# Kernel optimization log

Hardware: AMD Instinct MI355X
Metric: run time of the kernel (lower is better)

The kernel has to match this reference:

```python
import jax, jax.numpy as jnp
import numpy as np

D_IN, D_K, D_V, N_HEADS = 1024, 64, 64, 16
B, S = 4, 2048


def setup_inputs() -> dict:
    key = jax.random.key(0)
    ks = jax.random.split(key, 9)
    scale = 1.0 / np.sqrt(D_IN)
    return {
        "X": jax.random.normal(ks[0], (B, S, D_IN), dtype=jnp.float32),
        # per-head projection weights, stacked over heads: [H, d_in, d]
        "Wq": jax.random.normal(ks[1], (N_HEADS, D_IN, D_K), dtype=jnp.float32) * scale,
        "bq": jax.random.normal(ks[2], (N_HEADS, D_K), dtype=jnp.float32) * 0.02,
        "Wk": jax.random.normal(ks[3], (N_HEADS, D_IN, D_K), dtype=jnp.float32) * scale,
        "bk": jax.random.normal(ks[4], (N_HEADS, D_K), dtype=jnp.float32) * 0.02,
        "Wv": jax.random.normal(ks[5], (N_HEADS, D_IN, D_V), dtype=jnp.float32) * scale,
        "bv": jax.random.normal(ks[6], (N_HEADS, D_V), dtype=jnp.float32) * 0.02,
        # output projection: [H*d_v, d_in]
        "Wo": jax.random.normal(ks[7], (N_HEADS * D_V, D_IN), dtype=jnp.float32) * (1.0 / np.sqrt(N_HEADS * D_V)),
        "bo": jax.random.normal(ks[8], (D_IN,), dtype=jnp.float32) * 0.02,
    }


def reference(X, Wq, bq, Wk, bk, Wv, bv, Wo, bo):
    # Per-head linear projections, all heads batched: [B,H,S,d]
    Q = jnp.einsum('bsd,hdk->bhsk', X, Wq) + bq[None, :, None, :]
    K = jnp.einsum('bsd,hdk->bhsk', X, Wk) + bk[None, :, None, :]
    V = jnp.einsum('bsd,hdv->bhsv', X, Wv) + bv[None, :, None, :]

    d_k = Q.shape[-1]
    scores = jnp.einsum('bhsk,bhtk->bhst', Q, K) / jnp.sqrt(jnp.float32(d_k))

    S_len = X.shape[1]
    causal = jnp.tril(jnp.ones((S_len, S_len), dtype=bool))  # [S,S]
    scores = jnp.where(causal[None, None, :, :], scores, -jnp.inf)
    P = jax.nn.softmax(scores, axis=-1)

    A = jnp.einsum('bhst,bhtv->bhsv', P, V)        # [B,H,S,d_v]
    # concat heads along feature dim (head-major order matches torch cat over heads)
    A = A.transpose(0, 2, 1, 3).reshape(X.shape[0], S_len, -1)  # [B,S,H*d_v]
    return A @ Wo + bo
```

## Files before the change

### kernel.cpp

```cpp
#include <hip/hip_runtime.h>
#include <cstdint>
#include <cstddef>

typedef __attribute__((ext_vector_type(4))) float f32x4;
typedef __attribute__((ext_vector_type(8))) short s16x8;
typedef __attribute__((ext_vector_type(4))) short s16x4;
typedef __attribute__((ext_vector_type(4))) int i32x4;

#define DEV __device__ __forceinline__

DEV short f2bf(float f) {
    unsigned u = __builtin_bit_cast(unsigned, f);
    unsigned r = (u + 0x7FFFu + ((u >> 16) & 1u)) >> 16;
    return (short)r;
}

DEV void gload_lds16(const void* g, void* l) {
    __builtin_amdgcn_global_load_lds(
        (const __attribute__((address_space(1))) unsigned int*)g,
        (__attribute__((address_space(3))) unsigned int*)l, 16, 0, 0);
}


__global__ void k_cvt_x(const float* __restrict__ X, short* __restrict__ Xb, int n4) {
    int stride = gridDim.x * blockDim.x;
    for (int i = blockIdx.x * blockDim.x + threadIdx.x; i < n4; i += stride) {
        f32x4 v = *(const f32x4*)&X[i * 4];
        s16x4 s;
#pragma unroll
        for (int j = 0; j < 4; ++j) s[j] = f2bf(v[j]);
        *(s16x4*)&Xb[i * 4] = s;
    }
}

__global__ void k_pack_wqkv(const float* __restrict__ Wq, const float* __restrict__ Wk,
                            const float* __restrict__ Wv, short* __restrict__ Wbt, int n) {
    int stride = gridDim.x * blockDim.x;
    for (int o = blockIdx.x * blockDim.x + threadIdx.x; o < n; o += stride) {
        int c = o >> 10, d = o & 1023;
        int t = c >> 10, h = (c >> 6) & 15, k = c & 63;
        const float* W = (t == 0) ? Wq : (t == 1) ? Wk : Wv;
        Wbt[o] = f2bf(W[(h * 1024 + d) * 64 + k]);
    }
}

__global__ void k_pack_wo(const float* __restrict__ Wo, short* __restrict__ Wobt, int n) {
    int stride = gridDim.x * blockDim.x;
    for (int o = blockIdx.x * blockDim.x + threadIdx.x; o < n; o += stride) {
        int nn = o >> 10, c = o & 1023;
        Wobt[o] = f2bf(Wo[c * 1024 + nn]);
    }
}


template <int EPI>
__launch_bounds__(256)
__global__ void gemm_bf16(const short* __restrict__ Ag, const short* __restrict__ Btg,
                          const float* __restrict__ b0, const float* __restrict__ b1,
                          const float* __restrict__ b2,
                          short* __restrict__ O0, short* __restrict__ O1, short* __restrict__ O2,
                          float* __restrict__ Of) {
    __shared__ short As[128 * 64];
    __shared__ short Bs[128 * 64];
    const int tid = threadIdx.x;
    const int wave = tid >> 6, lane = tid & 63;
    const int wm = wave >> 1, wn = wave & 1;
    const int m0 = blockIdx.y * 128, n0 = blockIdx.x * 128;

    f32x4 acc[4][4] = {};

    const int lr = lane >> 3;
    const int cb = (lane & 7) * 16;
    const int cl = cb ^ (lr << 4);

    for (int kt = 0; kt < 16; ++kt) {
        __syncthreads();
#pragma unroll
        for (int i = 0; i < 4; ++i) {
            int r8 = wave * 32 + i * 8;
            const char* ga = (const char*)(Ag + (size_t)(m0 + r8 + lr) * 1024 + kt * 64) + cl;
            gload_lds16(ga, &As[r8 * 64]);
            const char* gb = (const char*)(Btg + (size_t)(n0 + r8 + lr) * 1024 + kt * 64) + cl;
            gload_lds16(gb, &Bs[r8 * 64]);
        }
        asm volatile("s_waitcnt vmcnt(0)" ::: "memory");
        __syncthreads();
#pragma unroll
        for (int ks = 0; ks < 2; ++ks) {
            int kb = ks * 64 + (lane >> 4) * 16;
            s16x8 af[4], bf[4];
#pragma unroll
            for (int mf = 0; mf < 4; ++mf) {
                int m = wm * 64 + mf * 16 + (lane & 15);
                af[mf] = *(const s16x8*)&As[m * 64 + ((kb ^ ((m & 7) << 4)) >> 1)];
            }
#pragma unroll
            for (int nf = 0; nf < 4; ++nf) {
                int n = wn * 64 + nf * 16 + (lane & 15);
                bf[nf] = *(const s16x8*)&Bs[n * 64 + ((kb ^ ((n & 7) << 4)) >> 1)];
            }
#pragma unroll
            for (int mf = 0; mf < 4; ++mf)
#pragma unroll
                for (int nf = 0; nf < 4; ++nf)
                    acc[mf][nf] = __builtin_amdgcn_mfma_f32_16x16x32_bf16(af[mf], bf[nf],
                                                                          acc[mf][nf], 0, 0, 0);
        }
    }

    if (EPI == 0) {
#pragma unroll
        for (int nf = 0; nf < 4; ++nf) {
            int n = n0 + wn * 64 + nf * 16 + (lane & 15);
            int t = n >> 10;
            int h = (n >> 6) & 15;
            int kk = n & 63;
            const float* bias = (t == 0) ? b0 : (t == 1) ? b1 : b2;
            short* dst = (t == 0) ? O0 : (t == 1) ? O1 : O2;
            float scale = (t == 0) ? 0.1803368851f : 1.0f;
            float bb = bias[h * 64 + kk];
#pragma unroll
            for (int mf = 0; mf < 4; ++mf) {
#pragma unroll
                for (int r = 0; r < 4; ++r) {
                    int m = m0 + wm * 64 + mf * 16 + (lane >> 4) * 4 + r;
                    int b_ = m >> 11, sp = m & 2047;
                    float v = (acc[mf][nf][r] + bb) * scale;
                    dst[(((size_t)(b_ * 16 + h)) * 2048 + sp) * 64 + kk] = f2bf(v);
                }
            }
        }
    } else {
#pragma unroll
        for (int nf = 0; nf < 4; ++nf) {
            int n = n0 + wn * 64 + nf * 16 + (lane & 15);
            float bb = b0[n];
#pragma unroll
            for (int mf = 0; mf < 4; ++mf) {
#pragma unroll
                for (int r = 0; r < 4; ++r) {
                    int m = m0 + wm * 64 + mf * 16 + (lane >> 4) * 4 + r;
                    Of[(size_t)m * 1024 + n] = acc[mf][nf][r] + bb;
                }
            }
        }
    }
}


#define STAGE_K(KT, OFF) do {                                                   \
    _Pragma("unroll")                                                           \
    for (int i_ = 0; i_ < 2; ++i_) {                                            \
        int l_ = wave * 16 + i_ * 8 + lr;          \
        int gr_ = (((l_ >> 4) & 1) << 5) | (((l_ >> 2) & 3) << 3) |             \
                  (((l_ >> 5) & 1) << 2) | (l_ & 3);        \
        const char* g_ = (const char*)(Kb + base + (size_t)((KT) * 64 + gr_) * 64) + cl; \
        gload_lds16(g_, &KsAll[(OFF) + (wave * 16 + i_ * 8) * 64]);             \
    } } while (0)

#define LOAD_V(KT, D0, D1) do {                                                 \
    const short* vs_ = Vb + base + (size_t)((KT) * 64 + 2 * kp) * 64 + vb8 * 8; \
    D0 = *(const s16x8*)vs_;                                                    \
    D1 = *(const s16x8*)(vs_ + 64); } while (0)

#define WRITE_V(OFF, S0, S1) do {                                               \
    _Pragma("unroll")                                                           \
    for (int j_ = 0; j_ < 8; ++j_) {                                            \
        int v_ = vb8 * 8 + j_;                                                  \
        unsigned pk_ = (unsigned)(unsigned short)S0[j_] |                       \
                       ((unsigned)(unsigned short)S1[j_] << 16);                \
        int bo_ = (4 * kp) ^ ((v_ & 7) << 4);                                   \
        *(unsigned*)((char*)&VtAll[(OFF) + v_ * 64] + bo_) = pk_;               \
    } } while (0)

#define STRIP2_COMPUTE(KT, OFF) do {                                            \
    f32x4 scL_[4], scS_[4];                                                     \
    _Pragma("unroll")                                                           \
    for (int nf_ = 0; nf_ < 4; ++nf_)                                           \
        _Pragma("unroll")                                                       \
        for (int r_ = 0; r_ < 4; ++r_) { scL_[nf_][r_] = -10.f; scS_[nf_][r_] = -10.f; } \
    __builtin_amdgcn_s_setprio(1);                                              \
    _Pragma("unroll")                                                           \
    for (int ks_ = 0; ks_ < 2; ++ks_) {                                         \
        int kb_ = ks_ * 64 + (lane >> 4) * 16;                                  \
        _Pragma("unroll")                                                       \
        for (int nf_ = 0; nf_ < 4; ++nf_) {                                     \
            int key_ = nf_ * 16 + (lane & 15);                                  \
            s16x8 bf_ = *(const s16x8*)&KsAll[(OFF) + key_ * 64 + ((kb_ ^ ((key_ & 7) << 4)) >> 1)]; \
            scL_[nf_] = __builtin_amdgcn_mfma_f32_16x16x32_bf16(bf_, qL_[ks_], scL_[nf_], 0, 0, 0); \
            scS_[nf_] = __builtin_amdgcn_mfma_f32_16x16x32_bf16(bf_, qS_[ks_], scS_[nf_], 0, 0, 0); \
        }                                                                       \
    }                                                                           \
    __builtin_amdgcn_s_setprio(0);                                              \
    if ((KT) == QTSv_) {                                   \
        int qq_ = wave * 16 + (lane & 15);                                      \
        int g8_ = (lane >> 4) * 8;                                              \
        _Pragma("unroll")                                                       \
        for (int nf_ = 0; nf_ < 4; ++nf_) {                                     \
            _Pragma("unroll")                                                   \
            for (int r_ = 0; r_ < 4; ++r_) {                                    \
                int key_ = ((nf_ & 1) << 5) + g8_ + ((nf_ >> 1) << 2) + r_;     \
                if (key_ > qq_) scS_[nf_][r_] = NEG_INF;                        \
            }                                                                   \
        }                                                                       \
    }                                                                           \
    _Pragma("unroll")                                                           \
    for (int nf_ = 0; nf_ < 4; ++nf_)                                           \
        _Pragma("unroll")                                                       \
        for (int r_ = 0; r_ < 4; ++r_) {                                        \
            scL_[nf_][r_] = exp2f(scL_[nf_][r_]);                               \
            scS_[nf_][r_] = exp2f(scS_[nf_][r_]);                               \
        }                                                                       \
    unsigned pdL_[4][2], pdS_[4][2];                                            \
    _Pragma("unroll")                                                           \
    for (int nf_ = 0; nf_ < 4; ++nf_) {                                         \
        asm("v_cvt_pk_bf16_f32 %0, %1, %2"                                      \
            : "=v"(pdL_[nf_][0]) : "v"(scL_[nf_][0]), "v"(scL_[nf_][1]));       \
        asm("v_cvt_pk_bf16_f32 %0, %1, %2"                                      \
            : "=v"(pdL_[nf_][1]) : "v"(scL_[nf_][2]), "v"(scL_[nf_][3]));       \
        asm("v_cvt_pk_bf16_f32 %0, %1, %2"                                      \
            : "=v"(pdS_[nf_][0]) : "v"(scS_[nf_][0]), "v"(scS_[nf_][1]));       \
        asm("v_cvt_pk_bf16_f32 %0, %1, %2"                                      \
            : "=v"(pdS_[nf_][1]) : "v"(scS_[nf_][2]), "v"(scS_[nf_][3]));       \
    }                                                                           \
    __builtin_amdgcn_s_setprio(1);                                              \
    _Pragma("unroll")                                                           \
    for (int ks_ = 0; ks_ < 2; ++ks_) {                                         \
        i32x4 piL_, piS_;                                                       \
        piL_[0] = (int)pdL_[ks_][0]; piL_[1] = (int)pdL_[ks_][1];               \
        piL_[2] = (int)pdL_[ks_ + 2][0]; piL_[3] = (int)pdL_[ks_ + 2][1];       \
        piS_[0] = (int)pdS_[ks_][0]; piS_[1] = (int)pdS_[ks_][1];               \
        piS_[2] = (int)pdS_[ks_ + 2][0]; piS_[3] = (int)pdS_[ks_ + 2][1];       \
        s16x8 paL_ = __builtin_bit_cast(s16x8, piL_);                           \
        s16x8 paS_ = __builtin_bit_cast(s16x8, piS_);                           \
        lsumL_ = __builtin_amdgcn_mfma_f32_16x16x32_bf16(paL_, onesf, lsumL_, 0, 0, 0); \
        lsumS_ = __builtin_amdgcn_mfma_f32_16x16x32_bf16(paS_, onesf, lsumS_, 0, 0, 0); \
        int kb_ = ks_ * 64 + (lane >> 4) * 16;                                  \
        _Pragma("unroll")                                                       \
        for (int nf_ = 0; nf_ < 4; ++nf_) {                                     \
            int v_ = nf_ * 16 + (lane & 15);                                    \
            s16x8 vf_ = *(const s16x8*)&VtAll[(OFF) + v_ * 64 + ((kb_ ^ ((v_ & 7) << 4)) >> 1)]; \
            oL_[nf_] = __builtin_amdgcn_mfma_f32_16x16x32_bf16(paL_, vf_, oL_[nf_], 0, 0, 0); \
            oS_[nf_] = __builtin_amdgcn_mfma_f32_16x16x32_bf16(paS_, vf_, oS_[nf_], 0, 0, 0); \
        }                                                                       \
    }                                                                           \
    __builtin_amdgcn_s_setprio(0);                                              \
    } while (0)

#define STRIP_COMPUTE(QF, O, LSUM, KT, OFF) do {                                \
    f32x4 sc_[4];                                                               \
    _Pragma("unroll")                                                           \
    for (int nf_ = 0; nf_ < 4; ++nf_)                                           \
        _Pragma("unroll")                                                       \
        for (int r_ = 0; r_ < 4; ++r_) sc_[nf_][r_] = -10.f;                    \
    __builtin_amdgcn_s_setprio(1);                                              \
    _Pragma("unroll")                                                           \
    for (int ks_ = 0; ks_ < 2; ++ks_) {                                         \
        int kb_ = ks_ * 64 + (lane >> 4) * 16;                                  \
        _Pragma("unroll")                                                       \
        for (int nf_ = 0; nf_ < 4; ++nf_) {                                     \
            int key_ = nf_ * 16 + (lane & 15);                                  \
            s16x8 bf_ = *(const s16x8*)&KsAll[(OFF) + key_ * 64 + ((kb_ ^ ((key_ & 7) << 4)) >> 1)]; \
            sc_[nf_] = __builtin_amdgcn_mfma_f32_16x16x32_bf16(bf_, QF[ks_], sc_[nf_], 0, 0, 0); \
        }                                                                       \
    }                                                                           \
    __builtin_amdgcn_s_setprio(0);                                              \
    {                                                                           \
        int qq_ = wave * 16 + (lane & 15);                                      \
        int g8_ = (lane >> 4) * 8;                                              \
        _Pragma("unroll")                                                       \
        for (int nf_ = 0; nf_ < 4; ++nf_) {                                     \
            _Pragma("unroll")                                                   \
            for (int r_ = 0; r_ < 4; ++r_) {                                    \
                int key_ = ((nf_ & 1) << 5) + g8_ + ((nf_ >> 1) << 2) + r_;     \
                if (key_ > qq_) sc_[nf_][r_] = NEG_INF;                         \
            }                                                                   \
        }                                                                       \
    }                                                                           \
    _Pragma("unroll")                                                           \
    for (int nf_ = 0; nf_ < 4; ++nf_)                                           \
        _Pragma("unroll")                                                       \
        for (int r_ = 0; r_ < 4; ++r_) sc_[nf_][r_] = exp2f(sc_[nf_][r_]);      \
    unsigned pd_[4][2];                                                         \
    _Pragma("unroll")                                                           \
    for (int nf_ = 0; nf_ < 4; ++nf_) {                                         \
        asm("v_cvt_pk_bf16_f32 %0, %1, %2"                                      \
            : "=v"(pd_[nf_][0]) : "v"(sc_[nf_][0]), "v"(sc_[nf_][1]));          \
        asm("v_cvt_pk_bf16_f32 %0, %1, %2"                                      \
            : "=v"(pd_[nf_][1]) : "v"(sc_[nf_][2]), "v"(sc_[nf_][3]));          \
    }                                                                           \
    __builtin_amdgcn_s_setprio(1);                                              \
    _Pragma("unroll")                                                           \
    for (int ks_ = 0; ks_ < 2; ++ks_) {                                         \
        i32x4 pi_;                                                              \
        pi_[0] = (int)pd_[ks_][0]; pi_[1] = (int)pd_[ks_][1];                   \
        pi_[2] = (int)pd_[ks_ + 2][0]; pi_[3] = (int)pd_[ks_ + 2][1];           \
        s16x8 pa_ = __builtin_bit_cast(s16x8, pi_);                             \
        LSUM = __builtin_amdgcn_mfma_f32_16x16x32_bf16(pa_, onesf, LSUM, 0, 0, 0); \
        int kb_ = ks_ * 64 + (lane >> 4) * 16;                                  \
        _Pragma("unroll")                                                       \
        for (int nf_ = 0; nf_ < 4; ++nf_) {                                     \
            int v_ = nf_ * 16 + (lane & 15);                                    \
            s16x8 vf_ = *(const s16x8*)&VtAll[(OFF) + v_ * 64 + ((kb_ ^ ((v_ & 7) << 4)) >> 1)]; \
            O[nf_] = __builtin_amdgcn_mfma_f32_16x16x32_bf16(pa_, vf_, O[nf_], 0, 0, 0); \
        }                                                                       \
    }                                                                           \
    __builtin_amdgcn_s_setprio(0);                                              \
    } while (0)

#define ITERB(T, L0, L1, W0, W1) do {                                           \
    const bool st_ = ((T) + 2 < ntp_);                                          \
    if (st_) { STAGE_K((T) + 2, off2_); LOAD_V((T) + 2, L0, L1); }              \
    STRIP2_COMPUTE((T), off0_);                                                 \
    WRITE_V(off1_, W0, W1);                                                     \
    if (st_) asm volatile("s_waitcnt vmcnt(4) lgkmcnt(0)" ::: "memory");        \
    else     asm volatile("s_waitcnt vmcnt(0) lgkmcnt(0)" ::: "memory");        \
    __builtin_amdgcn_s_barrier();                                               \
    int tmp_ = off0_; off0_ = off1_; off1_ = off2_; off2_ = tmp_;               \
} while (0)

#define EPILOGUE(QT, O, LSUM) do {                                              \
    _Pragma("unroll")                                                           \
    for (int r_ = 0; r_ < 4; ++r_) {                                            \
        float ld_ = 1.0f / LSUM[r_];                                            \
        int qr_ = wave * 16 + (lane >> 4) * 4 + r_;                             \
        _Pragma("unroll")                                                       \
        for (int nf_ = 0; nf_ < 4; ++nf_) {                                     \
            int col_ = h * 64 + nf_ * 16 + (lane & 15);                         \
            Ab[((size_t)(b_ * 2048 + (QT) * 64 + qr_)) * 1024 + col_] =         \
                f2bf(O[nf_][r_] * ld_);                                         \
        }                                                                       \
    } } while (0)

__launch_bounds__(256)
__global__ void attn_fwd(const short* __restrict__ Qb, const short* __restrict__ Kb,
                         const short* __restrict__ Vb, short* __restrict__ Ab) {
    __shared__ short KsAll[3 * 64 * 64];
    __shared__ short VtAll[3 * 64 * 64];
    const int tid = threadIdx.x, wave = tid >> 6, lane = tid & 63;
    const int hx = blockIdx.x;
    const int j = 15 - (int)blockIdx.y;
    const int QTLv_ = 2 * j + 1, QTSv_ = 2 * j;
    const int ntp_ = 2 * j + 2;
    const int NB_ = ntp_ - 1;
    const size_t base = (size_t)hx * 2048 * 64;
    const float NEG_INF = -__builtin_inff();
    const int b_ = hx >> 4, h = hx & 15;

    const int qrow = wave * 16 + (lane & 15);
    const int qoff = (lane >> 4) * 8;
    const int lr = lane >> 3, cl = ((lane & 7) * 16) ^ (lr << 4);
    const int kp = tid & 31;
    const int vb8 = tid >> 5;

    const s16x8 onesf = {(short)0x3F80, (short)0x3F80, (short)0x3F80, (short)0x3F80,
                         (short)0x3F80, (short)0x3F80, (short)0x3F80, (short)0x3F80};

    s16x8 qL_[2], qS_[2];
#pragma unroll
    for (int ks = 0; ks < 2; ++ks) {
        qL_[ks] = *(const s16x8*)&Qb[base + (size_t)(QTLv_ * 64 + qrow) * 64 + ks * 32 + qoff];
        qS_[ks] = *(const s16x8*)&Qb[base + (size_t)(QTSv_ * 64 + qrow) * 64 + ks * 32 + qoff];
    }

    f32x4 oL_[4] = {}, oS_[4] = {};
    f32x4 lsumL_ = {}, lsumS_ = {};
    s16x8 vA0_, vA1_, vB0_, vB1_;
    int off0_ = 0, off1_ = 4096, off2_ = 8192;

    STAGE_K(0, off0_); LOAD_V(0, vA0_, vA1_);
    STAGE_K(1, off1_); LOAD_V(1, vB0_, vB1_);
    WRITE_V(off0_, vA0_, vA1_);
    asm volatile("s_waitcnt vmcnt(4) lgkmcnt(0)" ::: "memory");
    __builtin_amdgcn_s_barrier();

    int t_ = 0;
    for (; t_ + 1 < NB_; t_ += 2) {
        ITERB(t_,     vA0_, vA1_, vB0_, vB1_);
        ITERB(t_ + 1, vB0_, vB1_, vA0_, vA1_);
    }
    if (t_ < NB_) { ITERB(t_, vA0_, vA1_, vB0_, vB1_); }

    STRIP_COMPUTE(qL_, oL_, lsumL_, QTLv_, off0_);

    EPILOGUE(QTLv_, oL_, lsumL_);
    EPILOGUE(QTSv_, oS_, lsumS_);
}


extern "C" void kernel_launch(void* const* d_in, const int* in_sizes, int n_in,
                              void* d_out, int out_size, void* d_ws, size_t ws_size,
                              hipStream_t stream) {
    const float* X  = (const float*)d_in[0];
    const float* Wq = (const float*)d_in[1];
    const float* bq = (const float*)d_in[2];
    const float* Wk = (const float*)d_in[3];
    const float* bk = (const float*)d_in[4];
    const float* Wv = (const float*)d_in[5];
    const float* bv = (const float*)d_in[6];
    const float* Wo = (const float*)d_in[7];
    const float* bo = (const float*)d_in[8];
    float* out = (float*)d_out;
    char* ws = (char*)d_ws;

    short* Xb   = (short*)(ws);
    short* Wbt  = (short*)(ws + 16777216);
    short* Wobt = (short*)(ws + 23068672);
    short* Qb   = (short*)(ws + 25165824);
    short* Kb   = (short*)(ws + 41943040);
    short* Vb   = (short*)(ws + 58720256);
    short* Ab   = (short*)(ws + 75497472);

    k_cvt_x<<<2048, 256, 0, stream>>>(X, Xb, 8192 * 1024 / 4);
    k_pack_wqkv<<<2048, 256, 0, stream>>>(Wq, Wk, Wv, Wbt, 3 * 1024 * 1024);
    k_pack_wo<<<1024, 256, 0, stream>>>(Wo, Wobt, 1024 * 1024);

    gemm_bf16<0><<<dim3(24, 64), 256, 0, stream>>>(Xb, Wbt, bq, bk, bv, Qb, Kb, Vb, nullptr);
    attn_fwd<<<dim3(64, 16), 256, 0, stream>>>(Qb, Kb, Vb, Ab);
    gemm_bf16<1><<<dim3(8, 64), 256, 0, stream>>>(Ab, Wobt, bo, nullptr, nullptr,
                                                  nullptr, nullptr, nullptr, out);
}
```

Measured before the change: 192.5 us.

## Reduce attention K/V pipeline from triple to double buffering

Switches the K/V shared-memory pipeline in the causal attention kernel from a three-stage ring with prefetch distance two to a two-stage ping-pong with prefetch distance one. LDS use per block drops by a third and fewer V registers are held across iterations, which may allow higher occupancy. In exchange, each iteration now waits for all outstanding global loads before writing V, so less load latency is hidden behind the QK/PV compute.

```diff
diff --git a/kernel.cpp b/kernel.cpp
--- a/kernel.cpp
+++ b/kernel.cpp
@@ -158,17 +158,17 @@
         gload_lds16(g_, &KsAll[(OFF) + (wave * 16 + i_ * 8) * 64]);             \
     } } while (0)
 
-#define LOAD_V(KT, D0, D1) do {                                                 \
+#define LOAD_V(KT) do {                                                         \
     const short* vs_ = Vb + base + (size_t)((KT) * 64 + 2 * kp) * 64 + vb8 * 8; \
-    D0 = *(const s16x8*)vs_;                                                    \
-    D1 = *(const s16x8*)(vs_ + 64); } while (0)
-
-#define WRITE_V(OFF, S0, S1) do {                                               \
+    v0_ = *(const s16x8*)vs_;                                                   \
+    v1_ = *(const s16x8*)(vs_ + 64); } while (0)
+
+#define WRITE_V(OFF) do {                                                       \
     _Pragma("unroll")                                                           \
     for (int j_ = 0; j_ < 8; ++j_) {                                            \
         int v_ = vb8 * 8 + j_;                                                  \
-        unsigned pk_ = (unsigned)(unsigned short)S0[j_] |                       \
-                       ((unsigned)(unsigned short)S1[j_] << 16);                \
+        unsigned pk_ = (unsigned)(unsigned short)v0_[j_] |                      \
+                       ((unsigned)(unsigned short)v1_[j_] << 16);               \
         int bo_ = (4 * kp) ^ ((v_ & 7) << 4);                                   \
         *(unsigned*)((char*)&VtAll[(OFF) + v_ * 64] + bo_) = pk_;               \
     } } while (0)
@@ -308,15 +308,15 @@
     __builtin_amdgcn_s_setprio(0);                                              \
     } while (0)
 
-#define ITERB(T, L0, L1, W0, W1) do {                                           \
-    const bool st_ = ((T) + 2 < ntp_);                                          \
-    if (st_) { STAGE_K((T) + 2, off2_); LOAD_V((T) + 2, L0, L1); }              \
+#define ITERB(T) do {                                                           \
+    STAGE_K((T) + 1, off1_);                                                    \
+    LOAD_V((T) + 1);                                                            \
     STRIP2_COMPUTE((T), off0_);                                                 \
-    WRITE_V(off1_, W0, W1);                                                     \
-    if (st_) asm volatile("s_waitcnt vmcnt(4) lgkmcnt(0)" ::: "memory");        \
-    else     asm volatile("s_waitcnt vmcnt(0) lgkmcnt(0)" ::: "memory");        \
+    asm volatile("s_waitcnt vmcnt(0)" ::: "memory");                            \
+    WRITE_V(off1_);                                                             \
+    asm volatile("s_waitcnt lgkmcnt(0)" ::: "memory");                          \
     __builtin_amdgcn_s_barrier();                                               \
-    int tmp_ = off0_; off0_ = off1_; off1_ = off2_; off2_ = tmp_;               \
+    int tmp_ = off0_; off0_ = off1_; off1_ = tmp_;                              \
 } while (0)
 
 #define EPILOGUE(QT, O, LSUM) do {                                              \
@@ -335,8 +335,8 @@
 __launch_bounds__(256)
 __global__ void attn_fwd(const short* __restrict__ Qb, const short* __restrict__ Kb,
                          const short* __restrict__ Vb, short* __restrict__ Ab) {
-    __shared__ short KsAll[3 * 64 * 64];
-    __shared__ short VtAll[3 * 64 * 64];
+    __shared__ short KsAll[2 * 64 * 64];
+    __shared__ short VtAll[2 * 64 * 64];
     const int tid = threadIdx.x, wave = tid >> 6, lane = tid & 63;
     const int hx = blockIdx.x;
     const int j = 15 - (int)blockIdx.y;
@@ -365,21 +365,19 @@
 
     f32x4 oL_[4] = {}, oS_[4] = {};
     f32x4 lsumL_ = {}, lsumS_ = {};
-    s16x8 vA0_, vA1_, vB0_, vB1_;
-    int off0_ = 0, off1_ = 4096, off2_ = 8192;
-
-    STAGE_K(0, off0_); LOAD_V(0, vA0_, vA1_);
-    STAGE_K(1, off1_); LOAD_V(1, vB0_, vB1_);
-    WRITE_V(off0_, vA0_, vA1_);
-    asm volatile("s_waitcnt vmcnt(4) lgkmcnt(0)" ::: "memory");
+    s16x8 v0_, v1_;
+    int off0_ = 0, off1_ = 4096;
+
+    STAGE_K(0, off0_);
+    LOAD_V(0);
+    asm volatile("s_waitcnt vmcnt(0)" ::: "memory");
+    WRITE_V(off0_);
+    asm volatile("s_waitcnt lgkmcnt(0)" ::: "memory");
     __builtin_amdgcn_s_barrier();
 
-    int t_ = 0;
-    for (; t_ + 1 < NB_; t_ += 2) {
-        ITERB(t_,     vA0_, vA1_, vB0_, vB1_);
-        ITERB(t_ + 1, vB0_, vB1_, vA0_, vA1_);
-    }
-    if (t_ < NB_) { ITERB(t_, vA0_, vA1_, vB0_, vB1_); }
+    for (int t_ = 0; t_ < NB_; ++t_) {
+        ITERB(t_);
+    }
 
     STRIP_COMPUTE(qL_, oL_, lsumL_, QTLv_, off0_);
 
```

After: 196.8 us. 2.2% more time.
